# Performance work log

Hardware: AMD Instinct MI355X
Metric: run time of the kernel (lower is better)

## Reference

```python
import jax, jax.numpy as jnp
import numpy as np

N_NODES = 50000
N_EDGES = 800000
D = 64
N_GRAPHS = 512
N_LAYERS = 3
HID_FC = 64
N_CLASSES = 10


def setup_inputs() -> dict:
    key = jax.random.key(0)
    ks = jax.random.split(key, 12)
    s = 1.0 / np.sqrt(D)
    x = jax.random.normal(ks[0], (N_NODES, D), dtype=jnp.float32)
    edge_index = jax.random.randint(ks[1], (2, N_EDGES), 0, N_NODES, dtype=jnp.int32)
    batch = jnp.sort(jax.random.randint(ks[2], (N_NODES,), 0, N_GRAPHS, dtype=jnp.int32))
    convW1 = jax.random.normal(ks[3], (N_LAYERS, D, D), dtype=jnp.float32) * s
    convb1 = jax.random.normal(ks[4], (N_LAYERS, D), dtype=jnp.float32) * 0.01
    convW2 = jax.random.normal(ks[5], (N_LAYERS, D, D), dtype=jnp.float32) * s
    convb2 = jax.random.normal(ks[6], (N_LAYERS, D), dtype=jnp.float32) * 0.01
    fcW1 = jax.random.normal(ks[7], (D, HID_FC), dtype=jnp.float32) * s
    fcb1 = jax.random.normal(ks[8], (HID_FC,), dtype=jnp.float32) * 0.01
    fcW2 = jax.random.normal(ks[9], (HID_FC, N_CLASSES), dtype=jnp.float32) * (1.0 / np.sqrt(HID_FC))
    fcb2 = jax.random.normal(ks[10], (N_CLASSES,), dtype=jnp.float32) * 0.01
    return {"x": x, "convW1": convW1, "convb1": convb1, "convW2": convW2,
            "convb2": convb2, "fcW1": fcW1, "fcb1": fcb1, "fcW2": fcW2,
            "fcb2": fcb2, "edge_index": edge_index, "batch": batch}


def reference(x, convW1, convb1, convW2, convb2, fcW1, fcb1, fcW2, fcb2, edge_index, batch):
    src, dst = edge_index[0], edge_index[1]
    h = x
    for l in range(N_LAYERS):
        # GIN aggregation: (1 + eps) * x + sum_{j in N(i)} x_j, eps = 0
        agg = jax.ops.segment_sum(h[src], dst, num_segments=N_NODES)
        h = h + agg
        # per-layer MLP: Linear -> ReLU -> Linear
        h = jax.nn.relu(h @ convW1[l] + convb1[l])
        h = h @ convW2[l] + convb2[l]
    # global max pool over nodes of each graph
    g = jax.ops.segment_max(h, batch, num_segments=N_GRAPHS)
    # FC head: Linear(64) -> ReLU -> Linear(num_classes)
    g = jax.nn.relu(g @ fcW1 + fcb1)
    logits = g @ fcW2 + fcb2
    return jax.nn.log_softmax(logits, axis=1)
```

## Files before the change

### kernel.cpp

```cpp
#include <hip/hip_runtime.h>
#include <math.h>

#define N_NODES 50000
#define N_EDGES 800000
#define D 64
#define N_GRAPHS 512
#define N_LAYERS 3
#define HID_FC 64
#define N_CLASSES 10

#define SCAN_B 512
#define NB_SCAN ((N_NODES + SCAN_B - 1) / SCAN_B)


__device__ __forceinline__ unsigned mapf(float f) {
  unsigned u = __float_as_uint(f);
  return (u & 0x80000000u) ? ~u : (u | 0x80000000u);
}
__device__ __forceinline__ float unmapf(unsigned u) {
  return __uint_as_float((u & 0x80000000u) ? (u & 0x7FFFFFFFu) : ~u);
}

__device__ __forceinline__ unsigned pack2(float a, float b) {
  unsigned ua = __float_as_uint(a);
  unsigned ub = __float_as_uint(b);
  ua += 0x7FFFu + ((ua >> 16) & 1u);
  ub += 0x7FFFu + ((ub >> 16) & 1u);
  return (ua >> 16) | (ub & 0xFFFF0000u);
}
__device__ __forceinline__ float2 unpack2(unsigned v) {
  return make_float2(__uint_as_float(v << 16), __uint_as_float(v & 0xFFFF0000u));
}


__global__ void to_bf16(const float* __restrict__ in, unsigned* __restrict__ out) {
  int i = blockIdx.x * 256 + threadIdx.x;
  float4 v = reinterpret_cast<const float4*>(in)[i];
  reinterpret_cast<uint2*>(out)[i] = make_uint2(pack2(v.x, v.y), pack2(v.z, v.w));
}


__global__ void hist_kernel(const int* __restrict__ dst, int* __restrict__ deg) {
  int e = blockIdx.x * 256 + threadIdx.x;
  if (e < N_EDGES) atomicAdd(&deg[dst[e]], 1);
}

__global__ void scan_blocks(const int* __restrict__ deg, int* __restrict__ bsum) {
  __shared__ int sd[SCAN_B];
  int i = blockIdx.x * SCAN_B + threadIdx.x;
  sd[threadIdx.x] = (i < N_NODES) ? deg[i] : 0;
  __syncthreads();
  for (int off = SCAN_B / 2; off > 0; off >>= 1) {
    if (threadIdx.x < off) sd[threadIdx.x] += sd[threadIdx.x + off];
    __syncthreads();
  }
  if (threadIdx.x == 0) bsum[blockIdx.x] = sd[0];
}

__global__ void scan_mid(int* __restrict__ bsum) {
  __shared__ int s[256];
  int t = threadIdx.x;
  if (t < NB_SCAN) s[t] = bsum[t];
  __syncthreads();
  if (t == 0) {
    int run = 0;
    for (int i = 0; i < NB_SCAN; ++i) { int v = s[i]; s[i] = run; run += v; }
  }
  __syncthreads();
  if (t < NB_SCAN) bsum[t] = s[t];
}

__global__ void scan_final(const int* __restrict__ deg, const int* __restrict__ bsum,
                           int* __restrict__ rs, int* __restrict__ cur) {
  __shared__ int sd[SCAN_B];
  int i = blockIdx.x * SCAN_B + threadIdx.x;
  int v = (i < N_NODES) ? deg[i] : 0;
  sd[threadIdx.x] = v;
  __syncthreads();
  for (int off = 1; off < SCAN_B; off <<= 1) {
    int add = (threadIdx.x >= off) ? sd[threadIdx.x - off] : 0;
    __syncthreads();
    sd[threadIdx.x] += add;
    __syncthreads();
  }
  if (i < N_NODES) {
    int ex = bsum[blockIdx.x] + sd[threadIdx.x] - v;
    rs[i] = ex;
    cur[i] = ex;
  }
  if (i == 0) rs[N_NODES] = N_EDGES;
}

__global__ void fill_csr(const int* __restrict__ src, const int* __restrict__ dst,
                         int* __restrict__ cur, int* __restrict__ csr) {
  int e = blockIdx.x * 256 + threadIdx.x;
  if (e >= N_EDGES) return;
  int p = atomicAdd(&cur[dst[e]], 1);
  csr[p] = src[e];
}


__global__ __launch_bounds__(256) void agg_bf16(
    const unsigned* __restrict__ hin, const int* __restrict__ csr,
    const int* __restrict__ rs, float* __restrict__ acc) {
  const int t = threadIdx.x;
  const int hw = t >> 5;
  const int hl = t & 31;
  const int node = blockIdx.x * 8 + hw;
  float2 a = unpack2(hin[node * 32 + hl]);
  int e = rs[node];
  const int e1 = rs[node + 1];
  for (; e + 4 <= e1; e += 4) {
    int s0 = csr[e], s1 = csr[e + 1], s2 = csr[e + 2], s3 = csr[e + 3];
    float2 v0 = unpack2(hin[s0 * 32 + hl]);
    float2 v1 = unpack2(hin[s1 * 32 + hl]);
    float2 v2 = unpack2(hin[s2 * 32 + hl]);
    float2 v3 = unpack2(hin[s3 * 32 + hl]);
    a.x += v0.x + v1.x; a.y += v0.y + v1.y;
    a.x += v2.x + v3.x; a.y += v2.y + v3.y;
  }
  for (; e < e1; ++e) {
    float2 v = unpack2(hin[csr[e] * 32 + hl]);
    a.x += v.x; a.y += v.y;
  }
  reinterpret_cast<float2*>(acc)[node * 32 + hl] = a;
}


template <int FINAL>
__global__ __launch_bounds__(256) void mlp64(
    const float* __restrict__ A,
    const float* __restrict__ W1, const float* __restrict__ b1,
    const float* __restrict__ W2, const float* __restrict__ b2,
    unsigned* __restrict__ hout,
    const int* __restrict__ batch, unsigned* __restrict__ gU) {
  __shared__ float Ws[64 * 64];
  __shared__ float As[16][68];
  __shared__ float Hs[16][68];
  const int t = threadIdx.x;
  const int r = t >> 4, cg = t & 15;
  const int row = blockIdx.x * 16 + r;

  {
    float4* ws = (float4*)Ws;
    const float4* wv = (const float4*)W1;
#pragma unroll
    for (int i = 0; i < 4; ++i) ws[t + 256 * i] = wv[t + 256 * i];
  }
  *(float4*)&As[r][cg * 4] = ((const float4*)(A + (size_t)row * 64))[cg];
  __syncthreads();

  float4 bb = ((const float4*)b1)[cg];
  float a0 = bb.x, a1 = bb.y, a2 = bb.z, a3 = bb.w;
#pragma unroll
  for (int k = 0; k < 64; ++k) {
    float x = As[r][k];
    float4 w = *(const float4*)&Ws[k * 64 + cg * 4];
    a0 = fmaf(x, w.x, a0);
    a1 = fmaf(x, w.y, a1);
    a2 = fmaf(x, w.z, a2);
    a3 = fmaf(x, w.w, a3);
  }
  Hs[r][cg * 4 + 0] = fmaxf(a0, 0.0f);
  Hs[r][cg * 4 + 1] = fmaxf(a1, 0.0f);
  Hs[r][cg * 4 + 2] = fmaxf(a2, 0.0f);
  Hs[r][cg * 4 + 3] = fmaxf(a3, 0.0f);
  __syncthreads();

  {
    float4* ws = (float4*)Ws;
    const float4* wv = (const float4*)W2;
#pragma unroll
    for (int i = 0; i < 4; ++i) ws[t + 256 * i] = wv[t + 256 * i];
  }
  __syncthreads();

  bb = ((const float4*)b2)[cg];
  a0 = bb.x; a1 = bb.y; a2 = bb.z; a3 = bb.w;
#pragma unroll
  for (int k = 0; k < 64; ++k) {
    float x = Hs[r][k];
    float4 w = *(const float4*)&Ws[k * 64 + cg * 4];
    a0 = fmaf(x, w.x, a0);
    a1 = fmaf(x, w.y, a1);
    a2 = fmaf(x, w.z, a2);
    a3 = fmaf(x, w.w, a3);
  }

  if (FINAL) {
    const int g = batch[row];
    atomicMax(&gU[g * 64 + cg * 4 + 0], mapf(a0));
    atomicMax(&gU[g * 64 + cg * 4 + 1], mapf(a1));
    atomicMax(&gU[g * 64 + cg * 4 + 2], mapf(a2));
    atomicMax(&gU[g * 64 + cg * 4 + 3], mapf(a3));
  } else {
    reinterpret_cast<uint2*>(hout)[row * 16 + cg] =
        make_uint2(pack2(a0, a1), pack2(a2, a3));
  }
}


__global__ void init_g(unsigned* __restrict__ gU) {
  int i = blockIdx.x * blockDim.x + threadIdx.x;
  if (i < N_GRAPHS * D) gU[i] = 0x007FFFFFu;
}

__global__ void head_kernel(const unsigned* __restrict__ gU,
                            const float* __restrict__ fcW1, const float* __restrict__ fcb1,
                            const float* __restrict__ fcW2, const float* __restrict__ fcb2,
                            float* __restrict__ out) {
  __shared__ float g[64];
  __shared__ float hid[64];
  __shared__ float logit[N_CLASSES];
  __shared__ float red[2];
  const int gi = blockIdx.x;
  const int t = threadIdx.x;

  g[t] = unmapf(gU[gi * D + t]);
  __syncthreads();

  float a = fcb1[t];
#pragma unroll
  for (int k = 0; k < 64; ++k) a = fmaf(g[k], fcW1[k * HID_FC + t], a);
  hid[t] = fmaxf(a, 0.0f);
  __syncthreads();

  if (t < N_CLASSES) {
    float l = fcb2[t];
#pragma unroll
    for (int k = 0; k < 64; ++k) l = fmaf(hid[k], fcW2[k * N_CLASSES + t], l);
    logit[t] = l;
  }
  __syncthreads();

  if (t == 0) {
    float m = logit[0];
    for (int i = 1; i < N_CLASSES; ++i) m = fmaxf(m, logit[i]);
    float s = 0.0f;
    for (int i = 0; i < N_CLASSES; ++i) s += expf(logit[i] - m);
    red[0] = m;
    red[1] = logf(s);
  }
  __syncthreads();

  if (t < N_CLASSES) out[gi * N_CLASSES + t] = logit[t] - red[0] - red[1];
}


extern "C" void kernel_launch(void* const* d_in, const int* in_sizes, int n_in,
                              void* d_out, int out_size, void* d_ws, size_t ws_size,
                              hipStream_t stream) {
  const float* x      = (const float*)d_in[0];
  const float* convW1 = (const float*)d_in[1];
  const float* convb1 = (const float*)d_in[2];
  const float* convW2 = (const float*)d_in[3];
  const float* convb2 = (const float*)d_in[4];
  const float* fcW1   = (const float*)d_in[5];
  const float* fcb1   = (const float*)d_in[6];
  const float* fcW2   = (const float*)d_in[7];
  const float* fcb2   = (const float*)d_in[8];
  const int*   edge   = (const int*)d_in[9];
  const int*   batch  = (const int*)d_in[10];
  float* out = (float*)d_out;

  const int* src = edge;
  const int* dst = edge + N_EDGES;

  unsigned* xb  = (unsigned*)d_ws;
  unsigned* hbA = xb + (size_t)N_NODES * 32;
  float*    acc = (float*)(hbA + (size_t)N_NODES * 32);
  unsigned* gU  = (unsigned*)(acc + (size_t)N_NODES * 64);
  int* rs  = (int*)(gU + N_GRAPHS * D);
  int* csr = rs + N_NODES + 1;
  int* deg  = (int*)acc;
  int* cur  = deg + N_NODES;
  int* bsum = cur + N_NODES;

  to_bf16<<<(N_NODES * 16) / 256, 256, 0, stream>>>(x, xb);
  init_g<<<(N_GRAPHS * D + 255) / 256, 256, 0, stream>>>(gU);

  hipMemsetAsync(deg, 0, N_NODES * sizeof(int), stream);
  hist_kernel<<<N_EDGES / 256, 256, 0, stream>>>(dst, deg);
  scan_blocks<<<NB_SCAN, SCAN_B, 0, stream>>>(deg, bsum);
  scan_mid<<<1, 256, 0, stream>>>(bsum);
  scan_final<<<NB_SCAN, SCAN_B, 0, stream>>>(deg, bsum, rs, cur);
  fill_csr<<<N_EDGES / 256, 256, 0, stream>>>(src, dst, cur, csr);

  const int AGG_B = N_NODES / 8;
  const int MLP_B = N_NODES / 16;
  agg_bf16<<<AGG_B, 256, 0, stream>>>(xb, csr, rs, acc);
  mlp64<0><<<MLP_B, 256, 0, stream>>>(acc, convW1, convb1, convW2, convb2,
                                      hbA, batch, gU);
  agg_bf16<<<AGG_B, 256, 0, stream>>>(hbA, csr, rs, acc);
  mlp64<0><<<MLP_B, 256, 0, stream>>>(acc, convW1 + D * D, convb1 + D,
                                      convW2 + D * D, convb2 + D, xb, batch, gU);
  agg_bf16<<<AGG_B, 256, 0, stream>>>(xb, csr, rs, acc);
  mlp64<1><<<MLP_B, 256, 0, stream>>>(acc, convW1 + 2 * D * D, convb1 + 2 * D,
                                      convW2 + 2 * D * D, convb2 + 2 * D,
                                      nullptr, batch, gU);

  head_kernel<<<N_GRAPHS, 64, 0, stream>>>(gU, fcW1, fcb1, fcW2, fcb2, out);
}
```

Measured before the change: 285.6 us.

## Use bf16x3 split MFMA for MLP and keep node features in fp32

The per-layer 64x64 MLP moves from scalar FMAs to 16x16x32 bf16 MFMA instructions. Activations and weights are split into hi/lo bf16 parts so three products recover near-fp32 accuracy, and the weights are pre-split once by a new prep kernel. Node features are now stored in fp32 rather than bf16, and the MLP writes its output back in place over the aggregation buffer. This removes the bf16 conversion kernel and the feature rounding, but it doubles the bytes gathered in each aggregation pass, which is likely the dominant cost.

Result: faster. 278.0 us (-2.7%).

```diff
diff --git a/kernel.cpp b/kernel.cpp
--- a/kernel.cpp
+++ b/kernel.cpp
@@ -5,12 +5,16 @@
 #define N_EDGES 800000
 #define D 64
 #define N_GRAPHS 512
-#define N_LAYERS 3
-#define HID_FC 64
 #define N_CLASSES 10
+#define NT 3125
 
 #define SCAN_B 512
 #define NB_SCAN ((N_NODES + SCAN_B - 1) / SCAN_B)
+
+typedef __attribute__((ext_vector_type(8))) short bf16x8;
+typedef __attribute__((ext_vector_type(4))) float f32x4;
+
+#define MFMA16(a, b, c) __builtin_amdgcn_mfma_f32_16x16x32_bf16(a, b, c, 0, 0, 0)
 
 
 __device__ __forceinline__ unsigned mapf(float f) {
@@ -20,23 +24,36 @@
 __device__ __forceinline__ float unmapf(unsigned u) {
   return __uint_as_float((u & 0x80000000u) ? (u & 0x7FFFFFFFu) : ~u);
 }
-
-__device__ __forceinline__ unsigned pack2(float a, float b) {
-  unsigned ua = __float_as_uint(a);
-  unsigned ub = __float_as_uint(b);
-  ua += 0x7FFFu + ((ua >> 16) & 1u);
-  ub += 0x7FFFu + ((ub >> 16) & 1u);
-  return (ua >> 16) | (ub & 0xFFFF0000u);
-}
-__device__ __forceinline__ float2 unpack2(unsigned v) {
-  return make_float2(__uint_as_float(v << 16), __uint_as_float(v & 0xFFFF0000u));
-}
-
-
-__global__ void to_bf16(const float* __restrict__ in, unsigned* __restrict__ out) {
-  int i = blockIdx.x * 256 + threadIdx.x;
-  float4 v = reinterpret_cast<const float4*>(in)[i];
-  reinterpret_cast<uint2*>(out)[i] = make_uint2(pack2(v.x, v.y), pack2(v.z, v.w));
+__device__ __forceinline__ ushort bf16_rne(float f) {
+  unsigned u = __float_as_uint(f);
+  u += 0x7FFFu + ((u >> 16) & 1u);
+  return (ushort)(u >> 16);
+}
+__device__ __forceinline__ float bf16_tof(ushort h) {
+  return __uint_as_float(((unsigned)h) << 16);
+}
+
+
+__global__ void wprep(const float* __restrict__ convW1, const float* __restrict__ convW2,
+                      ushort* __restrict__ wf) {
+  const int wi = blockIdx.x;
+  const int layer = wi >> 1, which = wi & 1;
+  const float* W = (which ? convW2 : convW1) + layer * 4096;
+  const int t = threadIdx.x;
+  const int f = t >> 6, lane = t & 63;
+  const int ct = f >> 1, ks = f & 1;
+  const int n = ct * 16 + (lane & 15);
+  const int k0 = ks * 32 + ((lane >> 4) << 3);
+  ushort hi[8], lo[8];
+#pragma unroll
+  for (int v = 0; v < 8; ++v) {
+    float w = W[(k0 + v) * 64 + n];
+    ushort h = bf16_rne(w);
+    hi[v] = h;
+    lo[v] = bf16_rne(w - bf16_tof(h));
+  }
+  *(uint4*)(wf + ((wi * 2 + 0) * 8 + f) * 512 + lane * 8) = *(uint4*)hi;
+  *(uint4*)(wf + ((wi * 2 + 1) * 8 + f) * 512 + lane * 8) = *(uint4*)lo;
 }
 
 
@@ -100,102 +117,151 @@
 }
 
 
-__global__ __launch_bounds__(256) void agg_bf16(
-    const unsigned* __restrict__ hin, const int* __restrict__ csr,
+__global__ __launch_bounds__(256) void agg_f32(
+    const float* __restrict__ hin, const int* __restrict__ csr,
     const int* __restrict__ rs, float* __restrict__ acc) {
   const int t = threadIdx.x;
-  const int hw = t >> 5;
-  const int hl = t & 31;
+  const int hw = t >> 5, hl = t & 31;
   const int node = blockIdx.x * 8 + hw;
-  float2 a = unpack2(hin[node * 32 + hl]);
+  const float2* __restrict__ H = (const float2*)hin;
+  float2 a = H[node * 32 + hl];
   int e = rs[node];
   const int e1 = rs[node + 1];
   for (; e + 4 <= e1; e += 4) {
     int s0 = csr[e], s1 = csr[e + 1], s2 = csr[e + 2], s3 = csr[e + 3];
-    float2 v0 = unpack2(hin[s0 * 32 + hl]);
-    float2 v1 = unpack2(hin[s1 * 32 + hl]);
-    float2 v2 = unpack2(hin[s2 * 32 + hl]);
-    float2 v3 = unpack2(hin[s3 * 32 + hl]);
+    float2 v0 = H[s0 * 32 + hl];
+    float2 v1 = H[s1 * 32 + hl];
+    float2 v2 = H[s2 * 32 + hl];
+    float2 v3 = H[s3 * 32 + hl];
     a.x += v0.x + v1.x; a.y += v0.y + v1.y;
     a.x += v2.x + v3.x; a.y += v2.y + v3.y;
   }
   for (; e < e1; ++e) {
-    float2 v = unpack2(hin[csr[e] * 32 + hl]);
+    float2 v = H[csr[e] * 32 + hl];
     a.x += v.x; a.y += v.y;
   }
-  reinterpret_cast<float2*>(acc)[node * 32 + hl] = a;
+  ((float2*)acc)[node * 32 + hl] = a;
 }
 
 
 template <int FINAL>
-__global__ __launch_bounds__(256) void mlp64(
-    const float* __restrict__ A,
-    const float* __restrict__ W1, const float* __restrict__ b1,
-    const float* __restrict__ W2, const float* __restrict__ b2,
-    unsigned* __restrict__ hout,
+__global__ __launch_bounds__(256) void mlp_mfma(
+    float* __restrict__ A,
+    const ushort* __restrict__ wfL,
+    const float* __restrict__ b1, const float* __restrict__ b2,
     const int* __restrict__ batch, unsigned* __restrict__ gU) {
-  __shared__ float Ws[64 * 64];
-  __shared__ float As[16][68];
-  __shared__ float Hs[16][68];
+  __shared__ char ldsraw[4][5504];
   const int t = threadIdx.x;
-  const int r = t >> 4, cg = t & 15;
-  const int row = blockIdx.x * 16 + r;
-
-  {
-    float4* ws = (float4*)Ws;
-    const float4* wv = (const float4*)W1;
-#pragma unroll
-    for (int i = 0; i < 4; ++i) ws[t + 256 * i] = wv[t + 256 * i];
-  }
-  *(float4*)&As[r][cg * 4] = ((const float4*)(A + (size_t)row * 64))[cg];
-  __syncthreads();
-
-  float4 bb = ((const float4*)b1)[cg];
-  float a0 = bb.x, a1 = bb.y, a2 = bb.z, a3 = bb.w;
-#pragma unroll
-  for (int k = 0; k < 64; ++k) {
-    float x = As[r][k];
-    float4 w = *(const float4*)&Ws[k * 64 + cg * 4];
-    a0 = fmaf(x, w.x, a0);
-    a1 = fmaf(x, w.y, a1);
-    a2 = fmaf(x, w.z, a2);
-    a3 = fmaf(x, w.w, a3);
-  }
-  Hs[r][cg * 4 + 0] = fmaxf(a0, 0.0f);
-  Hs[r][cg * 4 + 1] = fmaxf(a1, 0.0f);
-  Hs[r][cg * 4 + 2] = fmaxf(a2, 0.0f);
-  Hs[r][cg * 4 + 3] = fmaxf(a3, 0.0f);
-  __syncthreads();
-
-  {
-    float4* ws = (float4*)Ws;
-    const float4* wv = (const float4*)W2;
-#pragma unroll
-    for (int i = 0; i < 4; ++i) ws[t + 256 * i] = wv[t + 256 * i];
-  }
-  __syncthreads();
-
-  bb = ((const float4*)b2)[cg];
-  a0 = bb.x; a1 = bb.y; a2 = bb.z; a3 = bb.w;
-#pragma unroll
-  for (int k = 0; k < 64; ++k) {
-    float x = Hs[r][k];
-    float4 w = *(const float4*)&Ws[k * 64 + cg * 4];
-    a0 = fmaf(x, w.x, a0);
-    a1 = fmaf(x, w.y, a1);
-    a2 = fmaf(x, w.z, a2);
-    a3 = fmaf(x, w.w, a3);
+  const int w = t >> 6, lane = t & 63;
+  const int tile = blockIdx.x * 4 + w;
+  if (tile >= NT) return;
+  const int m = lane & 15, g = lane >> 4;
+  char* lds = ldsraw[w];
+
+  const float* Ar = A + (size_t)(tile * 16 + m) * 64;
+  bf16x8 aH[2], aL[2];
+#pragma unroll
+  for (int ks = 0; ks < 2; ++ks) {
+    float4 f0 = ((const float4*)Ar)[(ks * 32 + g * 8) >> 2];
+    float4 f1 = ((const float4*)Ar)[((ks * 32 + g * 8) >> 2) + 1];
+    float v[8] = {f0.x, f0.y, f0.z, f0.w, f1.x, f1.y, f1.z, f1.w};
+#pragma unroll
+    for (int e = 0; e < 8; ++e) {
+      ushort h = bf16_rne(v[e]);
+      aH[ks][e] = (short)h;
+      aL[ks][e] = (short)bf16_rne(v[e] - bf16_tof(h));
+    }
+  }
+
+  bf16x8 w1h[8], w1l[8];
+#pragma unroll
+  for (int f = 0; f < 8; ++f) {
+    w1h[f] = *(const bf16x8*)(wfL + f * 512 + lane * 8);
+    w1l[f] = *(const bf16x8*)(wfL + 4096 + f * 512 + lane * 8);
+  }
+
+  f32x4 acc1[4];
+#pragma unroll
+  for (int ct = 0; ct < 4; ++ct) {
+    f32x4 c = {0.f, 0.f, 0.f, 0.f};
+    c = MFMA16(aH[0], w1h[ct * 2 + 0], c);
+    c = MFMA16(aH[1], w1h[ct * 2 + 1], c);
+    c = MFMA16(aL[0], w1h[ct * 2 + 0], c);
+    c = MFMA16(aL[1], w1h[ct * 2 + 1], c);
+    c = MFMA16(aH[0], w1l[ct * 2 + 0], c);
+    c = MFMA16(aH[1], w1l[ct * 2 + 1], c);
+    acc1[ct] = c;
+  }
+
+  ushort* Hhi = (ushort*)lds;
+  ushort* Hlo = (ushort*)(lds + 2560);
+#pragma unroll
+  for (int ct = 0; ct < 4; ++ct) {
+    float bias = b1[ct * 16 + m];
+#pragma unroll
+    for (int j = 0; j < 4; ++j) {
+      float hv = fmaxf(acc1[ct][j] + bias, 0.f);
+      ushort hh = bf16_rne(hv);
+      int idx = (g * 4 + j) * 80 + ct * 16 + m;
+      Hhi[idx] = hh;
+      Hlo[idx] = bf16_rne(hv - bf16_tof(hh));
+    }
+  }
+
+  bf16x8 hH[2], hL[2];
+#pragma unroll
+  for (int ks = 0; ks < 2; ++ks) {
+    hH[ks] = *(const bf16x8*)(Hhi + m * 80 + ks * 32 + g * 8);
+    hL[ks] = *(const bf16x8*)(Hlo + m * 80 + ks * 32 + g * 8);
+  }
+
+  bf16x8 w2h[8], w2l[8];
+#pragma unroll
+  for (int f = 0; f < 8; ++f) {
+    w2h[f] = *(const bf16x8*)(wfL + 8192 + f * 512 + lane * 8);
+    w2l[f] = *(const bf16x8*)(wfL + 12288 + f * 512 + lane * 8);
+  }
+  f32x4 acc2[4];
+#pragma unroll
+  for (int ct = 0; ct < 4; ++ct) {
+    f32x4 c = {0.f, 0.f, 0.f, 0.f};
+    c = MFMA16(hH[0], w2h[ct * 2 + 0], c);
+    c = MFMA16(hH[1], w2h[ct * 2 + 1], c);
+    c = MFMA16(hL[0], w2h[ct * 2 + 0], c);
+    c = MFMA16(hL[1], w2h[ct * 2 + 1], c);
+    c = MFMA16(hH[0], w2l[ct * 2 + 0], c);
+    c = MFMA16(hH[1], w2l[ct * 2 + 1], c);
+    acc2[ct] = c;
   }
 
   if (FINAL) {
-    const int g = batch[row];
-    atomicMax(&gU[g * 64 + cg * 4 + 0], mapf(a0));
-    atomicMax(&gU[g * 64 + cg * 4 + 1], mapf(a1));
-    atomicMax(&gU[g * 64 + cg * 4 + 2], mapf(a2));
-    atomicMax(&gU[g * 64 + cg * 4 + 3], mapf(a3));
+    int b4[4];
+#pragma unroll
+    for (int j = 0; j < 4; ++j) b4[j] = batch[tile * 16 + g * 4 + j];
+#pragma unroll
+    for (int ct = 0; ct < 4; ++ct) {
+      float bias = b2[ct * 16 + m];
+#pragma unroll
+      for (int j = 0; j < 4; ++j) {
+        float v = acc2[ct][j] + bias;
+        atomicMax(&gU[b4[j] * 64 + ct * 16 + m], mapf(v));
+      }
+    }
   } else {
-    reinterpret_cast<uint2*>(hout)[row * 16 + cg] =
-        make_uint2(pack2(a0, a1), pack2(a2, a3));
+    float* O = (float*)lds;
+#pragma unroll
+    for (int ct = 0; ct < 4; ++ct) {
+      float bias = b2[ct * 16 + m];
+#pragma unroll
+      for (int j = 0; j < 4; ++j)
+        O[(g * 4 + j) * 84 + ct * 16 + m] = acc2[ct][j] + bias;
+    }
+    float* Aw = A + (size_t)(tile * 16 + m) * 64;
+#pragma unroll
+    for (int q = 0; q < 4; ++q) {
+      float4 vv = *(const float4*)(O + m * 84 + g * 16 + q * 4);
+      ((float4*)Aw)[g * 4 + q] = vv;
+    }
   }
 }
 
@@ -209,19 +275,19 @@
                             const float* __restrict__ fcW1, const float* __restrict__ fcb1,
                             const float* __restrict__ fcW2, const float* __restrict__ fcb2,
                             float* __restrict__ out) {
-  __shared__ float g[64];
+  __shared__ float gbuf[64];
   __shared__ float hid[64];
   __shared__ float logit[N_CLASSES];
   __shared__ float red[2];
   const int gi = blockIdx.x;
   const int t = threadIdx.x;
 
-  g[t] = unmapf(gU[gi * D + t]);
+  gbuf[t] = unmapf(gU[gi * D + t]);
   __syncthreads();
 
   float a = fcb1[t];
 #pragma unroll
-  for (int k = 0; k < 64; ++k) a = fmaf(g[k], fcW1[k * HID_FC + t], a);
+  for (int k = 0; k < 64; ++k) a = fmaf(gbuf[k], fcW1[k * 64 + t], a);
   hid[t] = fmaxf(a, 0.0f);
   __syncthreads();
 
@@ -234,11 +300,11 @@
   __syncthreads();
 
   if (t == 0) {
-    float m = logit[0];
-    for (int i = 1; i < N_CLASSES; ++i) m = fmaxf(m, logit[i]);
+    float mx = logit[0];
+    for (int i = 1; i < N_CLASSES; ++i) mx = fmaxf(mx, logit[i]);
     float s = 0.0f;
-    for (int i = 0; i < N_CLASSES; ++i) s += expf(logit[i] - m);
-    red[0] = m;
+    for (int i = 0; i < N_CLASSES; ++i) s += expf(logit[i] - mx);
+    red[0] = mx;
     red[1] = logf(s);
   }
   __syncthreads();
@@ -266,17 +332,17 @@
   const int* src = edge;
   const int* dst = edge + N_EDGES;
 
-  unsigned* xb  = (unsigned*)d_ws;
-  unsigned* hbA = xb + (size_t)N_NODES * 32;
-  float*    acc = (float*)(hbA + (size_t)N_NODES * 32);
-  unsigned* gU  = (unsigned*)(acc + (size_t)N_NODES * 64);
+  float* accA = (float*)d_ws;
+  float* accB = accA + (size_t)N_NODES * 64;
+  unsigned* gU = (unsigned*)(accB + (size_t)N_NODES * 64);
   int* rs  = (int*)(gU + N_GRAPHS * D);
   int* csr = rs + N_NODES + 1;
-  int* deg  = (int*)acc;
+  ushort* wf = (ushort*)(csr + N_EDGES);
+  int* deg  = (int*)accA;
   int* cur  = deg + N_NODES;
   int* bsum = cur + N_NODES;
 
-  to_bf16<<<(N_NODES * 16) / 256, 256, 0, stream>>>(x, xb);
+  wprep<<<6, 512, 0, stream>>>(convW1, convW2, wf);
   init_g<<<(N_GRAPHS * D + 255) / 256, 256, 0, stream>>>(gU);
 
   hipMemsetAsync(deg, 0, N_NODES * sizeof(int), stream);
@@ -287,17 +353,15 @@
   fill_csr<<<N_EDGES / 256, 256, 0, stream>>>(src, dst, cur, csr);
 
   const int AGG_B = N_NODES / 8;
-  const int MLP_B = N_NODES / 16;
-  agg_bf16<<<AGG_B, 256, 0, stream>>>(xb, csr, rs, acc);
-  mlp64<0><<<MLP_B, 256, 0, stream>>>(acc, convW1, convb1, convW2, convb2,
-                                      hbA, batch, gU);
-  agg_bf16<<<AGG_B, 256, 0, stream>>>(hbA, csr, rs, acc);
-  mlp64<0><<<MLP_B, 256, 0, stream>>>(acc, convW1 + D * D, convb1 + D,
-                                      convW2 + D * D, convb2 + D, xb, batch, gU);
-  agg_bf16<<<AGG_B, 256, 0, stream>>>(xb, csr, rs, acc);
-  mlp64<1><<<MLP_B, 256, 0, stream>>>(acc, convW1 + 2 * D * D, convb1 + 2 * D,
-                                      convW2 + 2 * D * D, convb2 + 2 * D,
-                                      nullptr, batch, gU);
+  const int MLP_B = (NT + 3) / 4;
+  agg_f32<<<AGG_B, 256, 0, stream>>>(x, csr, rs, accA);
+  mlp_mfma<0><<<MLP_B, 256, 0, stream>>>(accA, wf, convb1, convb2, batch, gU);
+  agg_f32<<<AGG_B, 256, 0, stream>>>(accA, csr, rs, accB);
+  mlp_mfma<0><<<MLP_B, 256, 0, stream>>>(accB, wf + 16384, convb1 + 64, convb2 + 64,
+                                         batch, gU);
+  agg_f32<<<AGG_B, 256, 0, stream>>>(accB, csr, rs, accA);
+  mlp_mfma<1><<<MLP_B, 256, 0, stream>>>(accA, wf + 32768, convb1 + 128, convb2 + 128,
+                                         batch, gU);
 
   head_kernel<<<N_GRAPHS, 64, 0, stream>>>(gU, fcW1, fcb1, fcW2, fcb2, out);
 }
```
